# Kernel tuning notes

Measured on AMD Instinct MI355X. Metric: run time of the kernel, lower is better.

The kernel has to match this reference:

```python
import jax, jax.numpy as jnp
import numpy as np

N_NODES = 50000
N_EDGES = 800000
N_GRAPHS = 256
F_IN = 75  # num_features_xd


def _lin_params(key, fan_in, fan_out):
    kw, kb = jax.random.split(key)
    s = 1.0 / np.sqrt(fan_in)
    W = jax.random.uniform(kw, (fan_in, fan_out), jnp.float32, -s, s)
    b = jax.random.uniform(kb, (fan_out,), jnp.float32, -s, s)
    return W, b


def setup_inputs() -> dict:
    key = jax.random.key(0)
    ks = jax.random.split(key, 8)
    x = jax.random.normal(ks[0], (N_NODES, F_IN), jnp.float32)
    edge_index = jax.random.randint(ks[1], (2, N_EDGES), 0, N_NODES, jnp.int32)
    batch = jnp.sort(jax.random.randint(ks[2], (N_NODES,), 0, N_GRAPHS, jnp.int32))
    W1, b1 = _lin_params(ks[3], F_IN, F_IN)            # conv1: 75 -> 75
    W2, b2 = _lin_params(ks[4], F_IN, 2 * F_IN)        # conv2: 75 -> 150
    W3, b3 = _lin_params(ks[5], 2 * F_IN, 4 * F_IN)    # conv3: 150 -> 300
    Wg1, bg1 = _lin_params(ks[6], 4 * F_IN, 1024)      # fc_g1: 300 -> 1024
    Wg2, bg2 = _lin_params(ks[7], 1024, 128)           # fc_g2: 1024 -> 128
    return dict(x=x, edge_index=edge_index, batch=batch,
                W1=W1, b1=b1, W2=W2, b2=b2, W3=W3, b3=b3,
                Wg1=Wg1, bg1=bg1, Wg2=Wg2, bg2=bg2)


def gcn_conv(x, W, b, src, dst, n):
    """PyG GCNConv: out = D^{-1/2}(A+I)D^{-1/2} X W + b (symmetric norm, self loops)."""
    h = x @ W                                   # [n, out]
    loop = jnp.arange(n, dtype=src.dtype)
    s = jnp.concatenate([src, loop])            # [E+n]
    d = jnp.concatenate([dst, loop])
    deg = jax.ops.segment_sum(jnp.ones(s.shape[0], x.dtype), d, num_segments=n)
    dinv = jnp.where(deg > 0, jax.lax.rsqrt(jnp.maximum(deg, 1e-12)), 0.0)
    norm = dinv[s] * dinv[d]                    # [E+n]
    out = jax.ops.segment_sum(norm[:, None] * h[s], d, num_segments=n)
    return out + b


def reference(x, edge_index, batch, W1, b1, W2, b2, W3, b3, Wg1, bg1, Wg2, bg2):
    src, dst = edge_index[0], edge_index[1]
    n = x.shape[0]
    h = jax.nn.relu(gcn_conv(x, W1, b1, src, dst, n))
    h = jax.nn.relu(gcn_conv(h, W2, b2, src, dst, n))
    h = jax.nn.relu(gcn_conv(h, W3, b3, src, dst, n))
    g = jax.ops.segment_max(h, batch, num_segments=N_GRAPHS)  # global max pool
    g = jax.nn.relu(g @ Wg1 + bg1)
    # dropout is identity in eval mode
    return g @ Wg2 + bg2
```

## Files before the change

kernel.cpp:

```cpp
#include <hip/hip_runtime.h>
#include <math.h>

#define SCAN_B 1024
#define LDST 40

typedef __attribute__((ext_vector_type(8))) short short8v;
typedef __attribute__((ext_vector_type(8))) unsigned short ushort8v;
typedef __attribute__((ext_vector_type(4))) float f32x4;

static inline int ceil_div_i(long long a, int b) { return (int)((a + b - 1) / b); }

__device__ __forceinline__ unsigned short f2bf(float x) {
    unsigned int u = __float_as_uint(x);
    u += 0x7fffu + ((u >> 16) & 1u);
    return (unsigned short)(u >> 16);
}
__device__ __forceinline__ float bf2f(unsigned short h) {
    return __uint_as_float(((unsigned int)h) << 16);
}


__global__ __launch_bounds__(256) void k_count(const int* __restrict__ dst, int E,
                                               int* __restrict__ cnt) {
    int i = blockIdx.x * blockDim.x + threadIdx.x;
    if (i < E) atomicAdd(&cnt[dst[i]], 1);
}

__global__ __launch_bounds__(256) void k_dinv(const int* __restrict__ cnt,
                                              float* __restrict__ dinv, int N) {
    int i = blockIdx.x * blockDim.x + threadIdx.x;
    if (i < N) dinv[i] = (float)(1.0 / sqrt((double)(cnt[i] + 1)));
}

__global__ __launch_bounds__(256) void k_scan1(const int* __restrict__ cnt,
                                               int* __restrict__ rowptr,
                                               int* __restrict__ bsum, int N) {
    __shared__ int s[256];
    int tid = threadIdx.x;
    int base = blockIdx.x * SCAN_B + tid * 4;
    int a0 = (base + 0 < N) ? cnt[base + 0] : 0;
    int a1 = (base + 1 < N) ? cnt[base + 1] : 0;
    int a2 = (base + 2 < N) ? cnt[base + 2] : 0;
    int a3 = (base + 3 < N) ? cnt[base + 3] : 0;
    int tsum = a0 + a1 + a2 + a3;
    s[tid] = tsum;
    __syncthreads();
    for (int off = 1; off < 256; off <<= 1) {
        int val = 0;
        if (tid >= off) val = s[tid - off];
        __syncthreads();
        if (tid >= off) s[tid] += val;
        __syncthreads();
    }
    int texcl = s[tid] - tsum;
    if (tid == 255) bsum[blockIdx.x] = s[255];
    if (base + 0 < N) rowptr[base + 0] = texcl;
    if (base + 1 < N) rowptr[base + 1] = texcl + a0;
    if (base + 2 < N) rowptr[base + 2] = texcl + a0 + a1;
    if (base + 3 < N) rowptr[base + 3] = texcl + a0 + a1 + a2;
}

__global__ __launch_bounds__(256) void k_scan2(int* __restrict__ bsum, int NB) {
    __shared__ int s[256];
    int tid = threadIdx.x;
    int v = (tid < NB) ? bsum[tid] : 0;
    s[tid] = v;
    __syncthreads();
    for (int off = 1; off < 256; off <<= 1) {
        int val = 0;
        if (tid >= off) val = s[tid - off];
        __syncthreads();
        if (tid >= off) s[tid] += val;
        __syncthreads();
    }
    if (tid < NB) bsum[tid] = s[tid] - v;
}

__global__ __launch_bounds__(256) void k_scan3(int* __restrict__ rowptr,
                                               const int* __restrict__ bsum, int N, int E) {
    int i = blockIdx.x * blockDim.x + threadIdx.x;
    if (i < N) rowptr[i] += bsum[i >> 10];
    if (i == 0) rowptr[N] = E;
}

__global__ __launch_bounds__(256) void k_fill(const int* __restrict__ src,
                                              const int* __restrict__ dst, int E,
                                              const int* __restrict__ rowptr,
                                              int* __restrict__ fill,
                                              const float* __restrict__ dinv,
                                              int* __restrict__ col,
                                              float* __restrict__ ew) {
    int e = blockIdx.x * blockDim.x + threadIdx.x;
    if (e >= E) return;
    int s = src[e], d = dst[e];
    int pos = atomicAdd(&fill[d], 1);
    int idx = rowptr[d] + pos;
    col[idx] = s;
    ew[idx] = dinv[s] * dinv[d];
}


__global__ __launch_bounds__(256) void k_xpad(const float* __restrict__ x,
                                              float* __restrict__ xp, int N, int F, int XS) {
    int i = blockIdx.x * blockDim.x + threadIdx.x;
    int v = i / XS, c = i - v * XS;
    if (v >= N) return;
    xp[i] = (c < F) ? x[(size_t)v * F + c] : 0.f;
}


template <int BF16IN, int UNR>
__global__ __launch_bounds__(256) void k_gather_v(const void* __restrict__ Xv,
                                                  const int* __restrict__ rowptr,
                                                  const int* __restrict__ col,
                                                  const float* __restrict__ ew,
                                                  const float* __restrict__ dinv,
                                                  float* __restrict__ T, int N,
                                                  int XS, int KPf) {
    const int v = blockIdx.x * 4 + (threadIdx.x >> 6);
    const int lane = threadIdx.x & 63;
    if (v >= N) return;
    const float dv = dinv[v];
    const float s = dv * dv;
    constexpr int VW = BF16IN ? 8 : 4;
    const int f0 = lane * VW;
    const bool act = f0 < XS;
    const float* Xf = (const float*)Xv;
    const unsigned short* Xb = (const unsigned short*)Xv;

    float acc[VW];
#pragma unroll
    for (int u = 0; u < VW; u++) acc[u] = 0.f;
    if (act) {
        if (BF16IN) {
            ushort8v h = *(const ushort8v*)(Xb + (size_t)v * XS + f0);
#pragma unroll
            for (int u = 0; u < VW; u++) acc[u] = s * bf2f(h[u]);
        } else {
            f32x4 t4 = *(const f32x4*)(Xf + (size_t)v * XS + f0);
#pragma unroll
            for (int u = 0; u < VW; u++) acc[u] = s * t4[u];
        }
    }

    const int beg = rowptr[v], end = rowptr[v + 1];
    for (int jb = beg; jb < end; jb += 64) {
        const int nj = min(64, end - jb);
        int ec = 0;
        float ev = 0.f;
        if (lane < nj) {
            ec = col[jb + lane];
            ev = ew[jb + lane];
        }
        int e = 0;
        for (; e + UNR <= nj; e += UNR) {
            int c[UNR];
            float w[UNR];
#pragma unroll
            for (int u = 0; u < UNR; u++) {
                c[u] = __shfl(ec, e + u);
                w[u] = __shfl(ev, e + u);
            }
            if (BF16IN) {
                ushort8v xv[UNR];
#pragma unroll
                for (int u = 0; u < UNR; u++)
                    if (act) xv[u] = *(const ushort8v*)(Xb + (size_t)c[u] * XS + f0);
#pragma unroll
                for (int u = 0; u < UNR; u++)
                    if (act) {
#pragma unroll
                        for (int k = 0; k < VW; k++)
                            acc[k] = fmaf(w[u], bf2f(xv[u][k]), acc[k]);
                    }
            } else {
                f32x4 xv[UNR];
#pragma unroll
                for (int u = 0; u < UNR; u++)
                    if (act) xv[u] = *(const f32x4*)(Xf + (size_t)c[u] * XS + f0);
#pragma unroll
                for (int u = 0; u < UNR; u++)
                    if (act) {
#pragma unroll
                        for (int k = 0; k < VW; k++)
                            acc[k] = fmaf(w[u], xv[u][k], acc[k]);
                    }
            }
        }
        for (; e + 2 <= nj; e += 2) {
            int c0 = __shfl(ec, e), c1 = __shfl(ec, e + 1);
            float w0 = __shfl(ev, e), w1 = __shfl(ev, e + 1);
            if (act) {
                if (BF16IN) {
                    ushort8v x0 = *(const ushort8v*)(Xb + (size_t)c0 * XS + f0);
                    ushort8v x1 = *(const ushort8v*)(Xb + (size_t)c1 * XS + f0);
#pragma unroll
                    for (int k = 0; k < VW; k++) {
                        acc[k] = fmaf(w0, bf2f(x0[k]), acc[k]);
                        acc[k] = fmaf(w1, bf2f(x1[k]), acc[k]);
                    }
                } else {
                    f32x4 x0 = *(const f32x4*)(Xf + (size_t)c0 * XS + f0);
                    f32x4 x1 = *(const f32x4*)(Xf + (size_t)c1 * XS + f0);
#pragma unroll
                    for (int k = 0; k < VW; k++) {
                        acc[k] = fmaf(w0, x0[k], acc[k]);
                        acc[k] = fmaf(w1, x1[k], acc[k]);
                    }
                }
            }
        }
        if (e < nj) {
            int c0 = __shfl(ec, e);
            float w0 = __shfl(ev, e);
            if (act) {
                if (BF16IN) {
                    ushort8v x0 = *(const ushort8v*)(Xb + (size_t)c0 * XS + f0);
#pragma unroll
                    for (int k = 0; k < VW; k++) acc[k] = fmaf(w0, bf2f(x0[k]), acc[k]);
                } else {
                    f32x4 x0 = *(const f32x4*)(Xf + (size_t)c0 * XS + f0);
#pragma unroll
                    for (int k = 0; k < VW; k++) acc[k] = fmaf(w0, x0[k], acc[k]);
                }
            }
        }
    }

    if (f0 < KPf) {
        float* tv = T + (size_t)v * KPf + f0;
        f32x4 o0 = {acc[0], acc[1], acc[2], acc[3]};
        *(f32x4*)tv = o0;
        if (VW == 8) {
            f32x4 o1 = {acc[4], acc[5], acc[6], acc[7]};
            *(f32x4*)(tv + 4) = o1;
        }
    }
}


__global__ __launch_bounds__(256) void k_wsplit(const float* __restrict__ W,
                                                unsigned short* __restrict__ Wth,
                                                unsigned short* __restrict__ Wtl,
                                                int K, int Fout, int KP) {
    int i = blockIdx.x * blockDim.x + threadIdx.x;
    if (i >= Fout * KP) return;
    int c = i / KP, k = i - c * KP;
    float w = (k < K) ? W[(size_t)k * Fout + c] : 0.f;
    unsigned short h = f2bf(w);
    Wth[i] = h;
    Wtl[i] = f2bf(w - bf2f(h));
}


template <int MODE>
__global__ __launch_bounds__(256) void k_gemm_mfma(
    const float* __restrict__ A, int KPf,
    const unsigned short* __restrict__ Bth, const unsigned short* __restrict__ Btl,
    const float* __restrict__ bias, unsigned short* __restrict__ Cb, int CSbf,
    const int* __restrict__ batch, float* __restrict__ G,
    int N, int KP, int Fout) {
    __shared__ unsigned short sAh[128 * LDST];
    __shared__ unsigned short sAl[128 * LDST];
    __shared__ unsigned short sBh[128 * LDST];
    __shared__ unsigned short sBl[128 * LDST];
    __shared__ int sBatch[128];

    const int t = threadIdx.x;
    const int r0 = blockIdx.x * 128;
    const int c0 = blockIdx.y * 128;
    const int lane = t & 63;
    const int wv = t >> 6;
    const int wrow = (wv >> 1) * 64;
    const int wcol = (wv & 1) * 64;
    const int l15 = lane & 15;
    const int lk = (lane >> 4) * 8;
    const int nt = KP >> 5;

    const int srow = t >> 1;
    const int sseg = (t & 1) << 4;

    if (MODE == 1 && t < 128) sBatch[t] = (r0 + t < N) ? batch[r0 + t] : -1;

    const bool arow_ok = (r0 + srow) < N;
    const bool bcol_ok = (c0 + srow) < Fout;
    const float* aRow = A + (size_t)(r0 + srow) * KPf;
    const unsigned short* bhRow = Bth + (size_t)(c0 + srow) * KP;
    const unsigned short* blRow = Btl + (size_t)(c0 + srow) * KP;

    float av[16];
    ushort8v rbh0, rbh1, rbl0, rbl1;

    auto gload = [&](int kk) {
#pragma unroll
        for (int u = 0; u < 4; u++) {
            int gk = kk + sseg + u * 4;
            f32x4 f = {0.f, 0.f, 0.f, 0.f};
            if (arow_ok && gk < KPf) f = *(const f32x4*)&aRow[gk];
#pragma unroll
            for (int e = 0; e < 4; e++) av[u * 4 + e] = f[e];
        }
        if (bcol_ok) {
            const ushort8v* p = (const ushort8v*)&bhRow[kk + sseg];
            rbh0 = p[0];
            rbh1 = p[1];
            p = (const ushort8v*)&blRow[kk + sseg];
            rbl0 = p[0];
            rbl1 = p[1];
        } else {
#pragma unroll
            for (int e = 0; e < 8; e++) { rbh0[e] = 0; rbh1[e] = 0; rbl0[e] = 0; rbl1[e] = 0; }
        }
    };

    auto wlds = [&]() {
        int off = srow * LDST + sseg;
        ushort8v h0, h1, l0, l1;
#pragma unroll
        for (int e = 0; e < 8; e++) {
            unsigned short hh = f2bf(av[e]);
            h0[e] = hh;
            l0[e] = f2bf(av[e] - bf2f(hh));
        }
#pragma unroll
        for (int e = 0; e < 8; e++) {
            unsigned short hh = f2bf(av[8 + e]);
            h1[e] = hh;
            l1[e] = f2bf(av[8 + e] - bf2f(hh));
        }
        *(ushort8v*)&sAh[off] = h0;
        *(ushort8v*)&sAh[off + 8] = h1;
        *(ushort8v*)&sAl[off] = l0;
        *(ushort8v*)&sAl[off + 8] = l1;
        *(ushort8v*)&sBh[off] = rbh0;
        *(ushort8v*)&sBh[off + 8] = rbh1;
        *(ushort8v*)&sBl[off] = rbl0;
        *(ushort8v*)&sBl[off + 8] = rbl1;
    };

    f32x4 acc[4][4];
#pragma unroll
    for (int i = 0; i < 4; i++)
#pragma unroll
        for (int j = 0; j < 4; j++) acc[i][j] = (f32x4){0.f, 0.f, 0.f, 0.f};

    gload(0);
    for (int tc = 0; tc < nt; ++tc) {
        wlds();
        __syncthreads();
        if (tc + 1 < nt) gload((tc + 1) * 32);
        short8v ah[4], al[4];
#pragma unroll
        for (int i = 0; i < 4; i++) {
            int ro = (wrow + i * 16 + l15) * LDST + lk;
            ah[i] = *(const short8v*)&sAh[ro];
            al[i] = *(const short8v*)&sAl[ro];
        }
#pragma unroll
        for (int j = 0; j < 4; j++) {
            int co = (wcol + j * 16 + l15) * LDST + lk;
            short8v bh = *(const short8v*)&sBh[co];
            short8v bl = *(const short8v*)&sBl[co];
#pragma unroll
            for (int i = 0; i < 4; i++) {
                acc[i][j] = __builtin_amdgcn_mfma_f32_16x16x32_bf16(al[i], bh, acc[i][j], 0, 0, 0);
                acc[i][j] = __builtin_amdgcn_mfma_f32_16x16x32_bf16(ah[i], bl, acc[i][j], 0, 0, 0);
                acc[i][j] = __builtin_amdgcn_mfma_f32_16x16x32_bf16(ah[i], bh, acc[i][j], 0, 0, 0);
            }
        }
        __syncthreads();
    }

    if (MODE == 0) {
#pragma unroll
        for (int j = 0; j < 4; j++) {
            int gc = c0 + wcol + j * 16 + l15;
            if (gc >= CSbf) continue;
            float bv = (gc < Fout) ? bias[gc] : 0.f;
#pragma unroll
            for (int i = 0; i < 4; i++) {
                int rb = r0 + wrow + i * 16 + (lane >> 4) * 4;
#pragma unroll
                for (int q = 0; q < 4; q++) {
                    int gr = rb + q;
                    if (gr >= N) continue;
                    float vv = (gc < Fout) ? fmaxf(acc[i][j][q] + bv, 0.f) : 0.f;
                    Cb[(size_t)gr * CSbf + gc] = f2bf(vv);
                }
            }
        }
    } else {
#pragma unroll
        for (int j = 0; j < 4; j++) {
            int gc = c0 + wcol + j * 16 + l15;
            if (gc >= Fout) continue;
            float bv = bias[gc];
            int gcur = -1;
            float vmax = 0.f;
#pragma unroll
            for (int i = 0; i < 4; i++) {
                int lr = wrow + i * 16 + (lane >> 4) * 4;
#pragma unroll
                for (int q = 0; q < 4; q++) {
                    int g = sBatch[lr + q];
                    float vv = fmaxf(acc[i][j][q] + bv, 0.f);
                    if (g < 0) continue;
                    if (g != gcur) {
                        if (gcur >= 0)
                            atomicMax((int*)&G[(size_t)gcur * Fout + gc], __float_as_int(vmax));
                        gcur = g;
                        vmax = vv;
                    } else {
                        vmax = fmaxf(vmax, vv);
                    }
                }
            }
            if (gcur >= 0) atomicMax((int*)&G[(size_t)gcur * Fout + gc], __float_as_int(vmax));
        }
    }
}


__global__ __launch_bounds__(256) void k_fc_lds(const float* __restrict__ A,
                                                const float* __restrict__ W,
                                                const float* __restrict__ bias,
                                                float* __restrict__ C,
                                                int M, int K, int Nout, int CTF, int do_relu) {
    extern __shared__ float sA[];
    const int t = threadIdx.x;
    const int NV = CTF >> 2;
    const int BM = 256 / NV;
    const int m0 = blockIdx.x * BM;
    const int cb = blockIdx.y * CTF;

    for (int i = t; i < BM * K; i += 256) {
        int r = i / K, k = i - r * K;
        int gm = m0 + r;
        sA[i] = (gm < M) ? A[(size_t)gm * K + k] : 0.f;
    }
    __syncthreads();

    const int ml = t / NV;
    const int oc = cb + (t - ml * NV) * 4;
    const int m = m0 + ml;
    if (m >= M) return;
    const float* a = sA + (size_t)ml * K;

    float4 acc = *(const float4*)&bias[oc];
    const int KM = K & ~7;
    int k = 0;
    for (; k < KM; k += 8) {
        float4 w[8];
#pragma unroll
        for (int u = 0; u < 8; u++)
            w[u] = *(const float4*)&W[(size_t)(k + u) * Nout + oc];
#pragma unroll
        for (int u = 0; u < 8; u++) {
            float avv = a[k + u];
            acc.x = fmaf(avv, w[u].x, acc.x);
            acc.y = fmaf(avv, w[u].y, acc.y);
            acc.z = fmaf(avv, w[u].z, acc.z);
            acc.w = fmaf(avv, w[u].w, acc.w);
        }
    }
    for (; k < K; k++) {
        float4 wv = *(const float4*)&W[(size_t)k * Nout + oc];
        float avv = a[k];
        acc.x = fmaf(avv, wv.x, acc.x);
        acc.y = fmaf(avv, wv.y, acc.y);
        acc.z = fmaf(avv, wv.z, acc.z);
        acc.w = fmaf(avv, wv.w, acc.w);
    }
    if (do_relu) {
        acc.x = fmaxf(acc.x, 0.f);
        acc.y = fmaxf(acc.y, 0.f);
        acc.z = fmaxf(acc.z, 0.f);
        acc.w = fmaxf(acc.w, 0.f);
    }
    *(float4*)&C[(size_t)m * Nout + oc] = acc;
}


extern "C" void kernel_launch(void* const* d_in, const int* in_sizes, int n_in,
                              void* d_out, int out_size, void* d_ws, size_t ws_size,
                              hipStream_t stream) {
    const float* x     = (const float*)d_in[0];
    const int*   ei    = (const int*)d_in[1];
    const int*   batch = (const int*)d_in[2];
    const float* W1 = (const float*)d_in[3];
    const float* b1 = (const float*)d_in[4];
    const float* W2 = (const float*)d_in[5];
    const float* b2 = (const float*)d_in[6];
    const float* W3 = (const float*)d_in[7];
    const float* b3 = (const float*)d_in[8];
    const float* Wg1 = (const float*)d_in[9];
    const float* bg1 = (const float*)d_in[10];
    const float* Wg2 = (const float*)d_in[11];
    const float* bg2 = (const float*)d_in[12];

    const int N  = in_sizes[2];
    const int E  = in_sizes[1] / 2;
    const int F1 = in_sizes[4];
    const int F2 = in_sizes[6];
    const int F3 = in_sizes[8];
    const int H1 = in_sizes[10];
    const int OC = in_sizes[12];
    const int NG = out_size / OC;
    const int FIN = in_sizes[3] / F1;

    const int KP1 = 96,  KPf1 = 80;
    const int KP3 = 160, KPf3 = 152;
    const int XSP = 76;
    const int HS1 = 80;
    const int HS2 = 152;

    const int* src = ei;
    const int* dst = ei + E;

    char* base = (char*)d_ws;
    size_t off = 0;
    auto alloc = [&](size_t bytes) -> void* {
        void* p = base + off;
        off = (off + bytes + 255) & ~(size_t)255;
        return p;
    };
    int*   cnt    = (int*)alloc((size_t)N * 4);
    int*   fill   = (int*)alloc((size_t)N * 4);
    int*   rowptr = (int*)alloc((size_t)(N + 1) * 4);
    float* dinv   = (float*)alloc((size_t)N * 4);
    int*   bsum   = (int*)alloc(256 * 4);
    int*   col    = (int*)alloc((size_t)E * 4);
    float* ew     = (float*)alloc((size_t)E * 4);
    unsigned short* W1th = (unsigned short*)alloc((size_t)F1 * KP1 * 2);
    unsigned short* W1tl = (unsigned short*)alloc((size_t)F1 * KP1 * 2);
    unsigned short* W2th = (unsigned short*)alloc((size_t)F2 * KP1 * 2);
    unsigned short* W2tl = (unsigned short*)alloc((size_t)F2 * KP1 * 2);
    unsigned short* W3th = (unsigned short*)alloc((size_t)F3 * KP3 * 2);
    unsigned short* W3tl = (unsigned short*)alloc((size_t)F3 * KP3 * 2);
    float* Gb  = (float*)alloc((size_t)NG * F3 * 4);
    float* g1  = (float*)alloc((size_t)NG * H1 * 4);
    float* Tg  = (float*)alloc((size_t)N * KPf3 * 4);
    float* xp  = (float*)alloc((size_t)N * XSP * 4);
    unsigned short* H1b = (unsigned short*)alloc((size_t)N * HS1 * 2);
    unsigned short* H2b = (unsigned short*)alloc((size_t)N * HS2 * 2);

    hipMemsetAsync(cnt, 0, (size_t)N * 4, stream);
    hipMemsetAsync(fill, 0, (size_t)N * 4, stream);
    hipMemsetAsync(Gb, 0, (size_t)NG * F3 * 4, stream);

    k_count<<<ceil_div_i(E, 256), 256, 0, stream>>>(dst, E, cnt);
    k_dinv<<<ceil_div_i(N, 256), 256, 0, stream>>>(cnt, dinv, N);
    int NB = ceil_div_i(N, SCAN_B);
    k_scan1<<<NB, 256, 0, stream>>>(cnt, rowptr, bsum, N);
    k_scan2<<<1, 256, 0, stream>>>(bsum, NB);
    k_scan3<<<ceil_div_i(N, 256), 256, 0, stream>>>(rowptr, bsum, N, E);
    k_fill<<<ceil_div_i(E, 256), 256, 0, stream>>>(src, dst, E, rowptr, fill, dinv, col, ew);

    k_wsplit<<<ceil_div_i((long long)F1 * KP1, 256), 256, 0, stream>>>(W1, W1th, W1tl, FIN, F1, KP1);
    k_wsplit<<<ceil_div_i((long long)F2 * KP1, 256), 256, 0, stream>>>(W2, W2th, W2tl, F1, F2, KP1);
    k_wsplit<<<ceil_div_i((long long)F3 * KP3, 256), 256, 0, stream>>>(W3, W3th, W3tl, F2, F3, KP3);
    k_xpad<<<ceil_div_i((long long)N * XSP, 256), 256, 0, stream>>>(x, xp, N, FIN, XSP);

    dim3 blk(256);
    int gw = ceil_div_i(N, 4);
    int gx = ceil_div_i(N, 128);

    k_gather_v<0, 8><<<gw, blk, 0, stream>>>(xp, rowptr, col, ew, dinv, Tg, N, XSP, KPf1);
    {
        dim3 g(gx, ceil_div_i(F1, 128));
        k_gemm_mfma<0><<<g, blk, 0, stream>>>(Tg, KPf1, W1th, W1tl, b1, H1b, HS1,
                                              nullptr, nullptr, N, KP1, F1);
    }
    k_gather_v<1, 8><<<gw, blk, 0, stream>>>(H1b, rowptr, col, ew, dinv, Tg, N, HS1, KPf1);
    {
        dim3 g(gx, ceil_div_i(F2, 128));
        k_gemm_mfma<0><<<g, blk, 0, stream>>>(Tg, KPf1, W2th, W2tl, b2, H2b, HS2,
                                              nullptr, nullptr, N, KP1, F2);
    }
    k_gather_v<1, 8><<<gw, blk, 0, stream>>>(H2b, rowptr, col, ew, dinv, Tg, N, HS2, KPf3);
    {
        dim3 g(gx, ceil_div_i(F3, 128));
        k_gemm_mfma<1><<<g, blk, 0, stream>>>(Tg, KPf3, W3th, W3tl, b3, nullptr, 0,
                                              batch, Gb, N, KP3, F3);
    }

    {
        int CTF = 256;
        int BM = 256 / (CTF / 4);
        dim3 g(ceil_div_i(NG, BM), H1 / CTF);
        size_t lds = (size_t)BM * F3 * 4;
        k_fc_lds<<<g, 256, lds, stream>>>(Gb, Wg1, bg1, g1, NG, F3, H1, CTF, 1);
    }
    {
        int CTF = OC;
        int BM = 256 / (CTF / 4);
        dim3 g(ceil_div_i(NG, BM), OC / CTF);
        size_t lds = (size_t)BM * H1 * 4;
        k_fc_lds<<<g, 256, lds, stream>>>(g1, Wg2, bg2, (float*)d_out, NG, H1, OC, CTF, 0);
    }
}
```

Baseline: 418.4 us.

## Split gather wavefronts into edge slots and restructure FC layers with split-K

```diff
diff --git a/kernel.cpp b/kernel.cpp
--- a/kernel.cpp
+++ b/kernel.cpp
@@ -109,8 +109,8 @@
 }
 
 
-template <int BF16IN, int UNR>
-__global__ __launch_bounds__(256) void k_gather_v(const void* __restrict__ Xv,
+template <int BF16IN, int CHUNKS, int SLOTS, int UNR>
+__global__ __launch_bounds__(256) void k_gather_s(const void* __restrict__ Xv,
                                                   const int* __restrict__ rowptr,
                                                   const int* __restrict__ col,
                                                   const float* __restrict__ ew,
@@ -120,18 +120,20 @@
     const int v = blockIdx.x * 4 + (threadIdx.x >> 6);
     const int lane = threadIdx.x & 63;
     if (v >= N) return;
+    constexpr int VW = BF16IN ? 8 : 4;
+    const int slot = lane / CHUNKS;
+    const int chunk = lane - slot * CHUNKS;
+    const bool act = lane < CHUNKS * SLOTS;
+    const int f0 = chunk * VW;
+    const float* Xf = (const float*)Xv;
+    const unsigned short* Xb = (const unsigned short*)Xv;
     const float dv = dinv[v];
     const float s = dv * dv;
-    constexpr int VW = BF16IN ? 8 : 4;
-    const int f0 = lane * VW;
-    const bool act = f0 < XS;
-    const float* Xf = (const float*)Xv;
-    const unsigned short* Xb = (const unsigned short*)Xv;
 
     float acc[VW];
 #pragma unroll
     for (int u = 0; u < VW; u++) acc[u] = 0.f;
-    if (act) {
+    if (slot == 0) {
         if (BF16IN) {
             ushort8v h = *(const ushort8v*)(Xb + (size_t)v * XS + f0);
 #pragma unroll
@@ -147,87 +149,62 @@
     for (int jb = beg; jb < end; jb += 64) {
         const int nj = min(64, end - jb);
         int ec = 0;
-        float ev = 0.f;
+        float emeta = 0.f;
         if (lane < nj) {
             ec = col[jb + lane];
-            ev = ew[jb + lane];
-        }
-        int e = 0;
-        for (; e + UNR <= nj; e += UNR) {
-            int c[UNR];
-            float w[UNR];
+            emeta = ew[jb + lane];
+        }
+        for (int e = 0; e < nj; e += SLOTS * UNR) {
+            int cs[UNR];
+            float ws[UNR];
+            bool vs[UNR];
 #pragma unroll
             for (int u = 0; u < UNR; u++) {
-                c[u] = __shfl(ec, e + u);
-                w[u] = __shfl(ev, e + u);
+                int srcl = e + u * SLOTS + slot;
+                vs[u] = act && (srcl < nj);
+                int sl = srcl & 63;
+                cs[u] = __shfl(ec, sl);
+                ws[u] = __shfl(emeta, sl);
+                if (!vs[u]) ws[u] = 0.f;
             }
             if (BF16IN) {
                 ushort8v xv[UNR];
 #pragma unroll
+                for (int u = 0; u < UNR; u++) {
+#pragma unroll
+                    for (int k2 = 0; k2 < 8; k2++) xv[u][k2] = 0;
+                    if (vs[u]) xv[u] = *(const ushort8v*)(Xb + (size_t)cs[u] * XS + f0);
+                }
+#pragma unroll
                 for (int u = 0; u < UNR; u++)
-                    if (act) xv[u] = *(const ushort8v*)(Xb + (size_t)c[u] * XS + f0);
-#pragma unroll
-                for (int u = 0; u < UNR; u++)
-                    if (act) {
-#pragma unroll
-                        for (int k = 0; k < VW; k++)
-                            acc[k] = fmaf(w[u], bf2f(xv[u][k]), acc[k]);
-                    }
+#pragma unroll
+                    for (int k2 = 0; k2 < VW; k2++)
+                        acc[k2] = fmaf(ws[u], bf2f(xv[u][k2]), acc[k2]);
             } else {
                 f32x4 xv[UNR];
 #pragma unroll
+                for (int u = 0; u < UNR; u++) {
+                    xv[u] = (f32x4){0.f, 0.f, 0.f, 0.f};
+                    if (vs[u]) xv[u] = *(const f32x4*)(Xf + (size_t)cs[u] * XS + f0);
+                }
+#pragma unroll
                 for (int u = 0; u < UNR; u++)
-                    if (act) xv[u] = *(const f32x4*)(Xf + (size_t)c[u] * XS + f0);
-#pragma unroll
-                for (int u = 0; u < UNR; u++)
-                    if (act) {
-#pragma unroll
-                        for (int k = 0; k < VW; k++)
-                            acc[k] = fmaf(w[u], xv[u][k], acc[k]);
-                    }
+#pragma unroll
+                    for (int k2 = 0; k2 < VW; k2++)
+                        acc[k2] = fmaf(ws[u], xv[u][k2], acc[k2]);
             }
         }
-        for (; e + 2 <= nj; e += 2) {
-            int c0 = __shfl(ec, e), c1 = __shfl(ec, e + 1);
-            float w0 = __shfl(ev, e), w1 = __shfl(ev, e + 1);
-            if (act) {
-                if (BF16IN) {
-                    ushort8v x0 = *(const ushort8v*)(Xb + (size_t)c0 * XS + f0);
-                    ushort8v x1 = *(const ushort8v*)(Xb + (size_t)c1 * XS + f0);
-#pragma unroll
-                    for (int k = 0; k < VW; k++) {
-                        acc[k] = fmaf(w0, bf2f(x0[k]), acc[k]);
-                        acc[k] = fmaf(w1, bf2f(x1[k]), acc[k]);
-                    }
-                } else {
-                    f32x4 x0 = *(const f32x4*)(Xf + (size_t)c0 * XS + f0);
-                    f32x4 x1 = *(const f32x4*)(Xf + (size_t)c1 * XS + f0);
-#pragma unroll
-                    for (int k = 0; k < VW; k++) {
-                        acc[k] = fmaf(w0, x0[k], acc[k]);
-                        acc[k] = fmaf(w1, x1[k], acc[k]);
-                    }
-                }
-            }
-        }
-        if (e < nj) {
-            int c0 = __shfl(ec, e);
-            float w0 = __shfl(ev, e);
-            if (act) {
-                if (BF16IN) {
-                    ushort8v x0 = *(const ushort8v*)(Xb + (size_t)c0 * XS + f0);
-#pragma unroll
-                    for (int k = 0; k < VW; k++) acc[k] = fmaf(w0, bf2f(x0[k]), acc[k]);
-                } else {
-                    f32x4 x0 = *(const f32x4*)(Xf + (size_t)c0 * XS + f0);
-#pragma unroll
-                    for (int k = 0; k < VW; k++) acc[k] = fmaf(w0, x0[k], acc[k]);
-                }
-            }
-        }
-    }
-
-    if (f0 < KPf) {
+    }
+
+#pragma unroll
+    for (int k2 = 0; k2 < VW; k2++) {
+        float t2 = acc[k2];
+#pragma unroll
+        for (int s2 = 1; s2 < SLOTS; s2++) t2 += __shfl(acc[k2], chunk + s2 * CHUNKS);
+        acc[k2] = t2;
+    }
+
+    if (slot == 0 && f0 < KPf) {
         float* tv = T + (size_t)v * KPf + f0;
         f32x4 o0 = {acc[0], acc[1], acc[2], acc[3]};
         *(f32x4*)tv = o0;
@@ -421,63 +398,86 @@
 }
 
 
-__global__ __launch_bounds__(256) void k_fc_lds(const float* __restrict__ A,
-                                                const float* __restrict__ W,
-                                                const float* __restrict__ bias,
-                                                float* __restrict__ C,
-                                                int M, int K, int Nout, int CTF, int do_relu) {
-    extern __shared__ float sA[];
+__global__ __launch_bounds__(256) void k_fc1(const float* __restrict__ A,
+                                             const float* __restrict__ W,
+                                             const float* __restrict__ bias,
+                                             float* __restrict__ C,
+                                             int M, int K, int Nout) {
+    __shared__ float sA[2 * 304];
     const int t = threadIdx.x;
-    const int NV = CTF >> 2;
-    const int BM = 256 / NV;
-    const int m0 = blockIdx.x * BM;
-    const int cb = blockIdx.y * CTF;
-
-    for (int i = t; i < BM * K; i += 256) {
+    const int m0 = blockIdx.x * 2;
+    const int oc = blockIdx.y * 256 + t;
+
+    for (int i = t; i < 2 * K; i += 256) {
         int r = i / K, k = i - r * K;
-        int gm = m0 + r;
-        sA[i] = (gm < M) ? A[(size_t)gm * K + k] : 0.f;
+        sA[r * 304 + k] = (m0 + r < M) ? A[(size_t)(m0 + r) * K + k] : 0.f;
     }
     __syncthreads();
 
-    const int ml = t / NV;
-    const int oc = cb + (t - ml * NV) * 4;
-    const int m = m0 + ml;
-    if (m >= M) return;
-    const float* a = sA + (size_t)ml * K;
-
-    float4 acc = *(const float4*)&bias[oc];
-    const int KM = K & ~7;
+    float acc0 = 0.f, acc1 = 0.f;
     int k = 0;
-    for (; k < KM; k += 8) {
-        float4 w[8];
-#pragma unroll
-        for (int u = 0; u < 8; u++)
-            w[u] = *(const float4*)&W[(size_t)(k + u) * Nout + oc];
+    for (; k + 8 <= K; k += 8) {
+        float w[8];
+#pragma unroll
+        for (int u = 0; u < 8; u++) w[u] = W[(size_t)(k + u) * Nout + oc];
 #pragma unroll
         for (int u = 0; u < 8; u++) {
-            float avv = a[k + u];
-            acc.x = fmaf(avv, w[u].x, acc.x);
-            acc.y = fmaf(avv, w[u].y, acc.y);
-            acc.z = fmaf(avv, w[u].z, acc.z);
-            acc.w = fmaf(avv, w[u].w, acc.w);
+            acc0 = fmaf(sA[k + u], w[u], acc0);
+            acc1 = fmaf(sA[304 + k + u], w[u], acc1);
         }
     }
     for (; k < K; k++) {
-        float4 wv = *(const float4*)&W[(size_t)k * Nout + oc];
-        float avv = a[k];
-        acc.x = fmaf(avv, wv.x, acc.x);
-        acc.y = fmaf(avv, wv.y, acc.y);
-        acc.z = fmaf(avv, wv.z, acc.z);
-        acc.w = fmaf(avv, wv.w, acc.w);
-    }
-    if (do_relu) {
-        acc.x = fmaxf(acc.x, 0.f);
-        acc.y = fmaxf(acc.y, 0.f);
-        acc.z = fmaxf(acc.z, 0.f);
-        acc.w = fmaxf(acc.w, 0.f);
-    }
-    *(float4*)&C[(size_t)m * Nout + oc] = acc;
+        float w = W[(size_t)k * Nout + oc];
+        acc0 = fmaf(sA[k], w, acc0);
+        acc1 = fmaf(sA[304 + k], w, acc1);
+    }
+    float bv = bias[oc];
+    if (m0 < M) C[(size_t)m0 * Nout + oc] = fmaxf(acc0 + bv, 0.f);
+    if (m0 + 1 < M) C[(size_t)(m0 + 1) * Nout + oc] = fmaxf(acc1 + bv, 0.f);
+}
+
+
+__global__ __launch_bounds__(256) void k_fc2p(const float* __restrict__ A,
+                                              const float* __restrict__ W,
+                                              float* __restrict__ P,
+                                              int M, int K, int Nout) {
+    __shared__ float sA[2 * 256];
+    const int t = threadIdx.x;
+    const int m0 = blockIdx.x * 2;
+    const int sk = blockIdx.y;
+    const int k0 = sk * 256;
+    const int row = t >> 7;
+    const int oc = t & 127;
+
+    for (int i = t; i < 2 * 256; i += 256) {
+        int r = i >> 8, k = i & 255;
+        sA[i] = (m0 + r < M) ? A[(size_t)(m0 + r) * K + k0 + k] : 0.f;
+    }
+    __syncthreads();
+
+    const float* a = sA + row * 256;
+    float acc = 0.f;
+    for (int k = 0; k < 256; k += 8) {
+        float w[8];
+#pragma unroll
+        for (int u = 0; u < 8; u++) w[u] = W[(size_t)(k0 + k + u) * Nout + oc];
+#pragma unroll
+        for (int u = 0; u < 8; u++) acc = fmaf(a[k + u], w[u], acc);
+    }
+    int m = m0 + row;
+    if (m < M) P[((size_t)sk * M + m) * Nout + oc] = acc;
+}
+
+__global__ __launch_bounds__(256) void k_fc2r(const float* __restrict__ P,
+                                              const float* __restrict__ bias,
+                                              float* __restrict__ C,
+                                              int M, int Nout, int SK) {
+    int i = blockIdx.x * blockDim.x + threadIdx.x;
+    if (i >= M * Nout) return;
+    int oc = i % Nout;
+    float acc = bias[oc];
+    for (int s2 = 0; s2 < SK; s2++) acc += P[(size_t)s2 * M * Nout + i];
+    C[i] = acc;
 }
 
 
@@ -539,6 +539,7 @@
     unsigned short* W3tl = (unsigned short*)alloc((size_t)F3 * KP3 * 2);
     float* Gb  = (float*)alloc((size_t)NG * F3 * 4);
     float* g1  = (float*)alloc((size_t)NG * H1 * 4);
+    float* P2  = (float*)alloc((size_t)4 * NG * OC * 4);
     float* Tg  = (float*)alloc((size_t)N * KPf3 * 4);
     float* xp  = (float*)alloc((size_t)N * XSP * 4);
     unsigned short* H1b = (unsigned short*)alloc((size_t)N * HS1 * 2);
@@ -565,19 +566,22 @@
     int gw = ceil_div_i(N, 4);
     int gx = ceil_div_i(N, 128);
 
-    k_gather_v<0, 8><<<gw, blk, 0, stream>>>(xp, rowptr, col, ew, dinv, Tg, N, XSP, KPf1);
+    k_gather_s<0, 19, 3, 4><<<gw, blk, 0, stream>>>(xp, rowptr, col, ew, dinv, Tg,
+                                                    N, XSP, KPf1);
     {
         dim3 g(gx, ceil_div_i(F1, 128));
         k_gemm_mfma<0><<<g, blk, 0, stream>>>(Tg, KPf1, W1th, W1tl, b1, H1b, HS1,
                                               nullptr, nullptr, N, KP1, F1);
     }
-    k_gather_v<1, 8><<<gw, blk, 0, stream>>>(H1b, rowptr, col, ew, dinv, Tg, N, HS1, KPf1);
+    k_gather_s<1, 10, 6, 2><<<gw, blk, 0, stream>>>(H1b, rowptr, col, ew, dinv, Tg,
+                                                    N, HS1, KPf1);
     {
         dim3 g(gx, ceil_div_i(F2, 128));
         k_gemm_mfma<0><<<g, blk, 0, stream>>>(Tg, KPf1, W2th, W2tl, b2, H2b, HS2,
                                               nullptr, nullptr, N, KP1, F2);
     }
-    k_gather_v<1, 8><<<gw, blk, 0, stream>>>(H2b, rowptr, col, ew, dinv, Tg, N, HS2, KPf3);
+    k_gather_s<1, 19, 3, 4><<<gw, blk, 0, stream>>>(H2b, rowptr, col, ew, dinv, Tg,
+                                                    N, HS2, KPf3);
     {
         dim3 g(gx, ceil_div_i(F3, 128));
         k_gemm_mfma<1><<<g, blk, 0, stream>>>(Tg, KPf3, W3th, W3tl, b3, nullptr, 0,
@@ -585,17 +589,13 @@
     }
 
     {
-        int CTF = 256;
-        int BM = 256 / (CTF / 4);
-        dim3 g(ceil_div_i(NG, BM), H1 / CTF);
-        size_t lds = (size_t)BM * F3 * 4;
-        k_fc_lds<<<g, 256, lds, stream>>>(Gb, Wg1, bg1, g1, NG, F3, H1, CTF, 1);
+        dim3 g(ceil_div_i(NG, 2), H1 / 256);
+        k_fc1<<<g, 256, 0, stream>>>(Gb, Wg1, bg1, g1, NG, F3, H1);
     }
     {
-        int CTF = OC;
-        int BM = 256 / (CTF / 4);
-        dim3 g(ceil_div_i(NG, BM), OC / CTF);
-        size_t lds = (size_t)BM * H1 * 4;
-        k_fc_lds<<<g, 256, lds, stream>>>(g1, Wg2, bg2, (float*)d_out, NG, H1, OC, CTF, 0);
-    }
-}
+        dim3 g(ceil_div_i(NG, 2), 4);
+        k_fc2p<<<g, 256, 0, stream>>>(g1, Wg2, P2, NG, H1, OC);
+        k_fc2r<<<ceil_div_i((long long)NG * OC, 256), 256, 0, stream>>>(
+            P2, bg2, (float*)d_out, NG, OC, 4);
+    }
+}
```

Result: faster. 356.6 us (-14.8%).
